# Performance work log

Hardware: AMD Instinct MI355X
Metric: run time of the kernel (lower is better)

Reference implementation:

```python
import jax, jax.numpy as jnp
import numpy as np

N, D, H, DFF, NH = 8192, 128, 256, 2048, 2
HD = D // NH
DEG = 32
E = N * DEG
LN_EPS = 1e-5


def setup_inputs() -> dict:
    key = jax.random.key(0)
    ks = jax.random.split(key, 20)
    s = 0.02
    return {
        "x": jax.random.normal(ks[0], (N, D), jnp.float32),
        "edge_index": jax.random.randint(ks[1], (2, E), 0, N, jnp.int64),
        "beta": jnp.ones((), jnp.float32),  # AGNNConv learnable beta, init 1
        "in_proj_w": jax.random.normal(ks[2], (3 * D, D), jnp.float32) * s,
        "in_proj_b": jnp.zeros((3 * D,), jnp.float32),
        "out_proj_w": jax.random.normal(ks[3], (D, D), jnp.float32) * s,
        "out_proj_b": jnp.zeros((D,), jnp.float32),
        "ln1_g": jnp.ones((D,), jnp.float32),
        "ln1_b": jnp.zeros((D,), jnp.float32),
        "ff1_w": jax.random.normal(ks[4], (DFF, D), jnp.float32) * s,
        "ff1_b": jnp.zeros((DFF,), jnp.float32),
        "ff2_w": jax.random.normal(ks[5], (D, DFF), jnp.float32) * s,
        "ff2_b": jnp.zeros((D,), jnp.float32),
        "ln2_g": jnp.ones((D,), jnp.float32),
        "ln2_b": jnp.zeros((D,), jnp.float32),
        "fc_w": jax.random.normal(ks[6], (H, D), jnp.float32) * s,
        "fc_b": jnp.zeros((H,), jnp.float32),
        "head_w": jax.random.normal(ks[7], (2, H), jnp.float32) * s,
        "head_b": jnp.zeros((2,), jnp.float32),
    }


def _layernorm(x, g, b):
    mu = jnp.mean(x, axis=-1, keepdims=True)
    var = jnp.mean((x - mu) ** 2, axis=-1, keepdims=True)
    return (x - mu) * jax.lax.rsqrt(var + LN_EPS) * g + b


def _agnn(x, edge_index, beta):
    # PyG AGNNConv: add self-loops, cosine-sim attention, segment softmax over targets
    n = x.shape[0]
    loop = jnp.arange(n, dtype=edge_index.dtype)
    src = jnp.concatenate([edge_index[0], loop])  # message source j
    dst = jnp.concatenate([edge_index[1], loop])  # aggregation target i
    xn = x / jnp.maximum(jnp.linalg.norm(x, axis=-1, keepdims=True), 1e-12)
    alpha = beta * jnp.sum(xn[dst] * xn[src], axis=-1)  # [E+N]
    m = jax.ops.segment_max(alpha, dst, num_segments=n)
    e = jnp.exp(alpha - m[dst])
    z = jax.ops.segment_sum(e, dst, num_segments=n)
    w = e / z[dst]
    return jax.ops.segment_sum(w[:, None] * x[src], dst, num_segments=n)


def reference(x, edge_index, beta, in_proj_w, in_proj_b, out_proj_w, out_proj_b,
              ln1_g, ln1_b, ff1_w, ff1_b, ff2_w, ff2_b, ln2_g, ln2_b,
              fc_w, fc_b, head_w, head_b):
    h = _agnn(x, edge_index, beta)  # [N, D]
    # transformer sees shape [N, 1, D] with batch_first=False -> seq over all N nodes
    qkv = h @ in_proj_w.T + in_proj_b  # [N, 3D]
    q, k, v = jnp.split(qkv, 3, axis=-1)
    q = q.reshape(N, NH, HD).transpose(1, 0, 2)  # [h, N, hd]
    k = k.reshape(N, NH, HD).transpose(1, 0, 2)
    v = v.reshape(N, NH, HD).transpose(1, 0, 2)
    scores = jnp.einsum('hnd,hmd->hnm', q, k) / jnp.sqrt(jnp.float32(HD))
    attn = jax.nn.softmax(scores, axis=-1)
    o = jnp.einsum('hnm,hmd->hnd', attn, v).transpose(1, 0, 2).reshape(N, D)
    o = o @ out_proj_w.T + out_proj_b
    h = _layernorm(h + o, ln1_g, ln1_b)  # post-LN (norm_first=False)
    ff = jax.nn.relu(h @ ff1_w.T + ff1_b) @ ff2_w.T + ff2_b
    h = _layernorm(h + ff, ln2_g, ln2_b)
    h = jax.nn.relu(h @ fc_w.T + fc_b)
    return h @ head_w.T + head_b  # [N, 2]
```

## Files before the change

kernel.cpp:

```cpp
#include <hip/hip_runtime.h>


typedef __attribute__((ext_vector_type(4))) float  f32x4;
typedef __attribute__((ext_vector_type(8))) __bf16 bf16x8;

#define DEV __device__ __forceinline__

DEV __bf16 f2bf(float f) {
  union { float f; unsigned u; } v; v.f = f;
  unsigned r = v.u + 0x7FFFu + ((v.u >> 16) & 1u);
  union { unsigned short s; __bf16 b; } o; o.s = (unsigned short)(r >> 16);
  return o.b;
}

DEV unsigned pk2(float a, float b) {
  union { float f; unsigned u; } x, y; x.f = a; y.f = b;
  unsigned ra = x.u + 0x7FFFu + ((x.u >> 16) & 1u);
  unsigned rb = y.u + 0x7FFFu + ((y.u >> 16) & 1u);
  return (ra >> 16) | (rb & 0xFFFF0000u);
}

DEV f32x4 mfma16(bf16x8 a, bf16x8 b, f32x4 c) {
  return __builtin_amdgcn_mfma_f32_16x16x32_bf16(a, b, c, 0, 0, 0);
}

#define GLD16(gp, lp) __builtin_amdgcn_global_load_lds(                        \
    (const __attribute__((address_space(1))) void*)(gp),                       \
    (__attribute__((address_space(3))) void*)(lp), 16, 0, 0)


__global__ __launch_bounds__(256) void k_norm(const float* __restrict__ x,
                                              float* __restrict__ inv) {
  int lane = threadIdx.x & 63, w = threadIdx.x >> 6;
  int row = blockIdx.x * 4 + w;
  float2 v = ((const float2*)(x + (size_t)row * 128))[lane];
  float s = v.x * v.x + v.y * v.y;
#pragma unroll
  for (int m = 1; m < 64; m <<= 1) s += __shfl_xor(s, m);
  if (lane == 0) inv[row] = 1.f / fmaxf(sqrtf(s), 1e-12f);
}

__global__ __launch_bounds__(256) void k_cvt5(
    const float* __restrict__ s0, const float* __restrict__ s1,
    const float* __restrict__ s2, const float* __restrict__ s3,
    const float* __restrict__ s4, __bf16* d0, __bf16* d1, __bf16* d2,
    __bf16* d3, __bf16* d4, int n0, int n1, int n2, int n3, int n4) {
  int t = blockIdx.x * 256 + threadIdx.x;
  if (t < n0) { d0[t] = f2bf(s0[t]); return; } t -= n0;
  if (t < n1) { d1[t] = f2bf(s1[t]); return; } t -= n1;
  if (t < n2) { d2[t] = f2bf(s2[t]); return; } t -= n2;
  if (t < n3) { d3[t] = f2bf(s3[t]); return; } t -= n3;
  if (t < n4) { d4[t] = f2bf(s4[t]); }
}

__global__ void k_count(const int* __restrict__ ei, int* __restrict__ counts,
                        int E) {
  int e = blockIdx.x * 256 + threadIdx.x;
  if (e < E) atomicAdd(&counts[ei[E + e]], 1);
}

__global__ __launch_bounds__(256) void k_scan(const int* __restrict__ counts,
                                              int* __restrict__ offs,
                                              int* __restrict__ cursor) {
  __shared__ int sums[256];
  int t = threadIdx.x, base = t * 32;
  int s = 0;
  for (int i = 0; i < 32; i++) s += counts[base + i];
  sums[t] = s;
  __syncthreads();
  for (int off = 1; off < 256; off <<= 1) {
    int v = (t >= off) ? sums[t - off] : 0;
    __syncthreads();
    sums[t] += v;
    __syncthreads();
  }
  int run = sums[t] - s;
  for (int i = 0; i < 32; i++) {
    offs[base + i] = run; cursor[base + i] = run;
    run += counts[base + i];
  }
  if (t == 255) offs[8192] = run;
}

__global__ void k_scatter(const int* __restrict__ ei, int* __restrict__ cursor,
                          int* __restrict__ csr, int E) {
  int e = blockIdx.x * 256 + threadIdx.x;
  if (e < E) {
    int dst = ei[E + e];
    int pos = atomicAdd(&cursor[dst], 1);
    csr[pos] = ei[e];
  }
}

__global__ __launch_bounds__(256) void k_agnn(
    const float* __restrict__ x, const int* __restrict__ csr,
    const int* __restrict__ offs, const float* __restrict__ inv,
    const float* __restrict__ betap, float* __restrict__ hf,
    __bf16* __restrict__ hb) {
  int lane = threadIdx.x & 63, w = threadIdx.x >> 6;
  int dst = blockIdx.x * 4 + w;
  float beta = *betap;
  float2 xd = ((const float2*)(x + (size_t)dst * 128))[lane];
  float invd = inv[dst];
  float sd = xd.x * xd.x + xd.y * xd.y;
#pragma unroll
  for (int m = 1; m < 64; m <<= 1) sd += __shfl_xor(sd, m);
  float z = __expf(beta * sd * invd * invd);
  float ax = z * xd.x, ay = z * xd.y;
  int e0 = offs[dst], e1 = offs[dst + 1];
  int e = e0;
  for (; e + 2 <= e1; e += 2) {
    int s0 = csr[e], s1 = csr[e + 1];
    float2 xa = ((const float2*)(x + (size_t)s0 * 128))[lane];
    float2 xb = ((const float2*)(x + (size_t)s1 * 128))[lane];
    float ia = inv[s0], ib = inv[s1];
    float da = xd.x * xa.x + xd.y * xa.y;
    float db = xd.x * xb.x + xd.y * xb.y;
#pragma unroll
    for (int m = 1; m < 64; m <<= 1) {
      da += __shfl_xor(da, m);
      db += __shfl_xor(db, m);
    }
    float sa = __expf(beta * da * invd * ia);
    float sb = __expf(beta * db * invd * ib);
    z += sa + sb;
    ax += sa * xa.x + sb * xb.x;
    ay += sa * xa.y + sb * xb.y;
  }
  if (e < e1) {
    int s0 = csr[e];
    float2 xa = ((const float2*)(x + (size_t)s0 * 128))[lane];
    float da = xd.x * xa.x + xd.y * xa.y;
#pragma unroll
    for (int m = 1; m < 64; m <<= 1) da += __shfl_xor(da, m);
    float sa = __expf(beta * da * invd * inv[s0]);
    z += sa; ax += sa * xa.x; ay += sa * xa.y;
  }
  float r = 1.f / z;
  ax *= r; ay *= r;
  float2 o; o.x = ax; o.y = ay;
  ((float2*)(hf + (size_t)dst * 128))[lane] = o;
  hb[(size_t)dst * 128 + 2 * lane]     = f2bf(ax);
  hb[(size_t)dst * 128 + 2 * lane + 1] = f2bf(ay);
}

__global__ __launch_bounds__(256, 2) void k_gemm(
    const __bf16* __restrict__ A, const __bf16* __restrict__ B,
    const float* __restrict__ bias, float* __restrict__ Cf,
    __bf16* __restrict__ Cb, float* __restrict__ Cpart, int M, int N, int K,
    int relu) {
  __shared__ __bf16 As[128 * 64];
  __shared__ __bf16 Bs[128 * 64];
  const int tid = threadIdx.x, lane = tid & 63, wid = tid >> 6;
  const int wm = wid & 1, wn = wid >> 1;
  const int bm = blockIdx.x * 128, bn = blockIdx.y * 128;
  const int kz = blockIdx.z, nkz = gridDim.z;
  const int kchunk = K / nkz, k0beg = kz * kchunk, k0end = k0beg + kchunk;
  const int lr = lane >> 3, lc8 = (lane & 7) * 8;
  const int l15 = lane & 15, quad = lane >> 4, kq = quad * 8;

  f32x4 acc[4][4] = {};
  const __bf16* Ab = A + (size_t)(bm + lr) * K + lc8;
  const __bf16* Bb = B + (size_t)(bn + lr) * K + lc8;

  for (int k0 = k0beg; k0 < k0end; k0 += 64) {
#pragma unroll
    for (int i = 0; i < 4; i++) {
      int j = wid * 4 + i;
      GLD16(Ab + (size_t)(8 * j) * K + k0, &As[j * 512]);
      GLD16(Bb + (size_t)(8 * j) * K + k0, &Bs[j * 512]);
    }
    __syncthreads();
    const int ar = (wm * 64 + l15) * 64 + kq;
    const int br = (wn * 64 + l15) * 64 + kq;
#pragma unroll
    for (int kk = 0; kk < 2; kk++) {
      bf16x8 a[4], b[4];
#pragma unroll
      for (int mt = 0; mt < 4; mt++)
        a[mt] = *(const bf16x8*)&As[ar + mt * 1024 + kk * 32];
#pragma unroll
      for (int nt = 0; nt < 4; nt++)
        b[nt] = *(const bf16x8*)&Bs[br + nt * 1024 + kk * 32];
#pragma unroll
      for (int mt = 0; mt < 4; mt++)
#pragma unroll
        for (int nt = 0; nt < 4; nt++)
          acc[mt][nt] = mfma16(a[mt], b[nt], acc[mt][nt]);
    }
    __syncthreads();
  }
  const int col0 = bn + wn * 64 + l15;
  const int row0 = bm + wm * 64 + quad * 4;
  if (Cpart) {
    float* P = Cpart + (size_t)kz * M * N;
#pragma unroll
    for (int mt = 0; mt < 4; mt++)
#pragma unroll
      for (int nt = 0; nt < 4; nt++)
#pragma unroll
        for (int r = 0; r < 4; r++)
          P[(size_t)(row0 + mt * 16 + r) * N + col0 + nt * 16] = acc[mt][nt][r];
  } else {
#pragma unroll
    for (int nt = 0; nt < 4; nt++) {
      float bv = bias[col0 + nt * 16];
#pragma unroll
      for (int mt = 0; mt < 4; mt++)
#pragma unroll
        for (int r = 0; r < 4; r++) {
          float v = acc[mt][nt][r] + bv;
          if (relu) v = fmaxf(v, 0.f);
          size_t idx = (size_t)(row0 + mt * 16 + r) * N + col0 + nt * 16;
          if (Cf) Cf[idx] = v;
          if (Cb) Cb[idx] = f2bf(v);
        }
    }
  }
}

__global__ __launch_bounds__(256) void k_qkvprep(const float* __restrict__ qkv,
                                                 __bf16* __restrict__ Qb,
                                                 __bf16* __restrict__ Kb,
                                                 __bf16* __restrict__ Vtb) {
  __shared__ __bf16 tile[64][130];
  int nb = blockIdx.x * 64;
  int t = threadIdx.x;
  for (int rr = 0; rr < 64; rr++) {
    int row = nb + rr;
    float v = qkv[(size_t)row * 384 + t];
    if (t < 128) {
      Qb[((size_t)(t >> 6) * 8192 + row) * 64 + (t & 63)] = f2bf(v * 0.125f);
    } else {
      int c = t - 128;
      Kb[((size_t)(c >> 6) * 8192 + row) * 64 + (c & 63)] = f2bf(v);
    }
  }
  int col = t & 127, rh = t >> 7;
  for (int rr = 0; rr < 64; rr += 2) {
    int row = rr + rh;
    tile[row][col] = f2bf(qkv[(size_t)(nb + row) * 384 + 256 + col]);
  }
  __syncthreads();
  int hd = t >> 1, half = t & 1;
  __bf16 tmp[32];
#pragma unroll
  for (int i = 0; i < 32; i++) tmp[i] = tile[half * 32 + i][hd];
  __bf16* dst = Vtb + (size_t)hd * 8192 + nb + half * 32;
#pragma unroll
  for (int i = 0; i < 4; i++)
    *(bf16x8*)(dst + i * 8) = *(const bf16x8*)(tmp + i * 8);
}

__global__ __launch_bounds__(256, 4) void k_attn(
    const __bf16* __restrict__ Qb, const __bf16* __restrict__ Kb,
    const __bf16* __restrict__ Vtb, float* __restrict__ Opart,
    float* __restrict__ Lpart) {
  __shared__ __bf16 Ks[4096];
  __shared__ __bf16 Vs[4096];
  __shared__ __bf16 Ps[4][32 * 88];

  const int tid = threadIdx.x, lane = tid & 63, w = tid >> 6;
  const int qt = blockIdx.x, h = blockIdx.y, kz = blockIdx.z;
  const int qbase = qt * 128;
  const int l15 = lane & 15, quad = lane >> 4;
  const int lofs = lane * 8;

  const __bf16* Qg = Qb + ((size_t)h * 8192 + qbase) * 64;
  const __bf16* Kg = Kb + (size_t)h * 8192 * 64;
  const __bf16* Vg = Vtb + (size_t)h * 64 * 8192;

#pragma unroll
  for (int i = 0; i < 2; i++) {
    int j = w * 2 + i;
    __bf16* dstb = (j < 4) ? &Ks[j * 1024] : &Vs[(j - 4) * 1024];
#pragma unroll
    for (int hh = 0; hh < 2; hh++)
      GLD16(Qg + (size_t)(j * 16 + l15) * 64 + hh * 32 + quad * 8,
            dstb + hh * 512);
  }
  __syncthreads();
  bf16x8 aq[2][2];
#pragma unroll
  for (int s = 0; s < 2; s++) {
    int j = w * 2 + s;
    const __bf16* base = (j < 4) ? &Ks[j * 1024] : &Vs[(j - 4) * 1024];
    aq[s][0] = *(const bf16x8*)&base[lofs];
    aq[s][1] = *(const bf16x8*)&base[512 + lofs];
  }
  __syncthreads();

  f32x4 o[2][4] = {};
  float lsum[2] = {0.f, 0.f};
  const int kstart = kz * 1024;

  for (int kt = 0; kt < 16; kt++) {
    int kb = kstart + kt * 64;
#pragma unroll
    for (int hh = 0; hh < 2; hh++) {
      GLD16(Kg + (size_t)(kb + w * 16 + l15) * 64 + hh * 32 + quad * 8,
            &Ks[w * 1024 + hh * 512]);
      GLD16(Vg + (size_t)(w * 16 + l15) * 8192 + kb + hh * 32 + quad * 8,
            &Vs[w * 1024 + hh * 512]);
    }
    __syncthreads();

#pragma unroll
    for (int mt = 0; mt < 4; mt++) {
      bf16x8 k0 = *(const bf16x8*)&Ks[mt * 1024 + lofs];
      bf16x8 k1 = *(const bf16x8*)&Ks[mt * 1024 + 512 + lofs];
#pragma unroll
      for (int s = 0; s < 2; s++) {
        f32x4 St = {};
        St = mfma16(k0, aq[s][0], St);
        St = mfma16(k1, aq[s][1], St);
        float p0 = __expf(St[0]), p1 = __expf(St[1]);
        float p2 = __expf(St[2]), p3 = __expf(St[3]);
        lsum[s] += (p0 + p1) + (p2 + p3);
        uint2 pk;
        pk.x = pk2(p0, p1);
        pk.y = pk2(p2, p3);
        *(uint2*)&Ps[w][(s * 16 + l15) * 88 + mt * 16 + quad * 4] = pk;
      }
    }
#pragma unroll
    for (int s = 0; s < 2; s++) {
      bf16x8 ap0 = *(const bf16x8*)&Ps[w][(s * 16 + l15) * 88 + quad * 8];
      bf16x8 ap1 = *(const bf16x8*)&Ps[w][(s * 16 + l15) * 88 + 32 + quad * 8];
#pragma unroll
      for (int nd = 0; nd < 4; nd++) {
        bf16x8 v0 = *(const bf16x8*)&Vs[nd * 1024 + lofs];
        bf16x8 v1 = *(const bf16x8*)&Vs[nd * 1024 + 512 + lofs];
        o[s][nd] = mfma16(ap0, v0, o[s][nd]);
        o[s][nd] = mfma16(ap1, v1, o[s][nd]);
      }
    }
    __syncthreads();
  }

#pragma unroll
  for (int s = 0; s < 2; s++) {
    float v = lsum[s];
    v += __shfl_xor(v, 16);
    v += __shfl_xor(v, 32);
    lsum[s] = v;
  }

  const size_t bpart = (size_t)(h * 8 + kz);
#pragma unroll
  for (int s = 0; s < 2; s++) {
#pragma unroll
    for (int nd = 0; nd < 4; nd++)
#pragma unroll
      for (int r = 0; r < 4; r++) {
        int row = qbase + w * 32 + s * 16 + quad * 4 + r;
        Opart[(bpart * 8192 + row) * 64 + nd * 16 + l15] = o[s][nd][r];
      }
    if (lane < 16) {
      int row = qbase + w * 32 + s * 16 + l15;
      Lpart[bpart * 8192 + row] = lsum[s];
    }
  }
}

__global__ __launch_bounds__(256) void k_attn_combine(
    const float* __restrict__ Opart, const float* __restrict__ Lpart,
    __bf16* __restrict__ obf) {
  int t = blockIdx.x * 256 + threadIdx.x;
  int d = t & 63;
  int n = (t >> 6) & 8191;
  int h = t >> 19;
  float acc = 0.f, L = 0.f;
#pragma unroll
  for (int z = 0; z < 8; z++) {
    size_t idx = (size_t)(h * 8 + z) * 8192 + n;
    acc += Opart[idx * 64 + d];
    L += Lpart[idx];
  }
  obf[(size_t)n * 128 + h * 64 + d] = f2bf(acc / L);
}

__global__ __launch_bounds__(256) void k_addln(
    const float* __restrict__ A, const float* __restrict__ Bv,
    const float* __restrict__ g, const float* __restrict__ bt,
    float* __restrict__ outf, __bf16* __restrict__ outb) {
  int lane = threadIdx.x & 63, w = threadIdx.x >> 6;
  int row = blockIdx.x * 4 + w;
  float2 a = ((const float2*)(A + (size_t)row * 128))[lane];
  float2 b = ((const float2*)(Bv + (size_t)row * 128))[lane];
  float vx = a.x + b.x, vy = a.y + b.y;
  float s = vx + vy;
#pragma unroll
  for (int m = 1; m < 64; m <<= 1) s += __shfl_xor(s, m);
  float mu = s * (1.f / 128.f);
  float dx = vx - mu, dy = vy - mu;
  float q = dx * dx + dy * dy;
#pragma unroll
  for (int m = 1; m < 64; m <<= 1) q += __shfl_xor(q, m);
  float rstd = rsqrtf(q * (1.f / 128.f) + 1e-5f);
  float2 gg = ((const float2*)g)[lane];
  float2 bb = ((const float2*)bt)[lane];
  float y0 = dx * rstd * gg.x + bb.x;
  float y1 = dy * rstd * gg.y + bb.y;
  if (outf) {
    float2 o; o.x = y0; o.y = y1;
    ((float2*)(outf + (size_t)row * 128))[lane] = o;
  }
  if (outb) {
    outb[(size_t)row * 128 + 2 * lane]     = f2bf(y0);
    outb[(size_t)row * 128 + 2 * lane + 1] = f2bf(y1);
  }
}

__global__ __launch_bounds__(256) void k_addln4(
    const float* __restrict__ A, const float* __restrict__ part,
    const float* __restrict__ pbias, const float* __restrict__ g,
    const float* __restrict__ bt, __bf16* __restrict__ outb) {
  int lane = threadIdx.x & 63, w = threadIdx.x >> 6;
  int row = blockIdx.x * 4 + w;
  float2 a = ((const float2*)(A + (size_t)row * 128))[lane];
  float2 pb = ((const float2*)pbias)[lane];
  float sx = 0.f, sy = 0.f;
#pragma unroll
  for (int z = 0; z < 4; z++) {
    float2 p =
        ((const float2*)(part + (size_t)z * 1048576 + (size_t)row * 128))[lane];
    sx += p.x; sy += p.y;
  }
  float vx = a.x + pb.x + sx, vy = a.y + pb.y + sy;
  float s = vx + vy;
#pragma unroll
  for (int m = 1; m < 64; m <<= 1) s += __shfl_xor(s, m);
  float mu = s * (1.f / 128.f);
  float dx = vx - mu, dy = vy - mu;
  float q = dx * dx + dy * dy;
#pragma unroll
  for (int m = 1; m < 64; m <<= 1) q += __shfl_xor(q, m);
  float rstd = rsqrtf(q * (1.f / 128.f) + 1e-5f);
  float2 gg = ((const float2*)g)[lane];
  float2 bb = ((const float2*)bt)[lane];
  outb[(size_t)row * 128 + 2 * lane]     = f2bf(dx * rstd * gg.x + bb.x);
  outb[(size_t)row * 128 + 2 * lane + 1] = f2bf(dy * rstd * gg.y + bb.y);
}

__global__ __launch_bounds__(256) void k_head(const float* __restrict__ fc,
                                              const float* __restrict__ hw,
                                              const float* __restrict__ hb,
                                              float* __restrict__ out) {
  int lane = threadIdx.x & 63, w = threadIdx.x >> 6;
  int row = blockIdx.x * 4 + w;
  float4 v  = ((const float4*)(fc + (size_t)row * 256))[lane];
  float4 w0 = ((const float4*)hw)[lane];
  float4 w1 = ((const float4*)(hw + 256))[lane];
  float p0 = v.x * w0.x + v.y * w0.y + v.z * w0.z + v.w * w0.w;
  float p1 = v.x * w1.x + v.y * w1.y + v.z * w1.z + v.w * w1.w;
#pragma unroll
  for (int m = 1; m < 64; m <<= 1) {
    p0 += __shfl_xor(p0, m);
    p1 += __shfl_xor(p1, m);
  }
  if (lane == 0) {
    out[(size_t)row * 2]     = p0 + hb[0];
    out[(size_t)row * 2 + 1] = p1 + hb[1];
  }
}

extern "C" void kernel_launch(void* const* d_in, const int* in_sizes, int n_in,
                              void* d_out, int out_size, void* d_ws,
                              size_t ws_size, hipStream_t stream) {
  const float* x     = (const float*)d_in[0];
  const int*   ei    = (const int*)d_in[1];
  const float* beta  = (const float*)d_in[2];
  const float* in_w  = (const float*)d_in[3];
  const float* in_b  = (const float*)d_in[4];
  const float* out_w = (const float*)d_in[5];
  const float* out_b = (const float*)d_in[6];
  const float* ln1g  = (const float*)d_in[7];
  const float* ln1b  = (const float*)d_in[8];
  const float* ff1w  = (const float*)d_in[9];
  const float* ff1b  = (const float*)d_in[10];
  const float* ff2w  = (const float*)d_in[11];
  const float* ff2b  = (const float*)d_in[12];
  const float* ln2g  = (const float*)d_in[13];
  const float* ln2b  = (const float*)d_in[14];
  const float* fcw   = (const float*)d_in[15];
  const float* fcb   = (const float*)d_in[16];
  const float* hw    = (const float*)d_in[17];
  const float* hbias = (const float*)d_in[18];
  float* out = (float*)d_out;
  const int N = 8192;
  const int E = in_sizes[1] / 2;

  char* wsp = (char*)d_ws;
  size_t off = 0;
  auto alloc = [&](size_t b) -> void* {
    void* p = wsp + off;
    off = (off + b + 255) & ~(size_t)255;
    return p;
  };

  float*  inv     = (float*)alloc((size_t)N * 4);
  int*    counts  = (int*)alloc((size_t)N * 4);
  int*    offs    = (int*)alloc((size_t)(N + 1) * 4);
  int*    cursor  = (int*)alloc((size_t)N * 4);
  int*    csr     = (int*)alloc((size_t)E * 4);
  float*  h_f     = (float*)alloc((size_t)N * 128 * 4);
  __bf16* h_b     = (__bf16*)alloc((size_t)N * 128 * 2);
  __bf16* o_b     = (__bf16*)alloc((size_t)N * 128 * 2);
  float*  oproj   = (float*)alloc((size_t)N * 128 * 4);
  float*  h1_f    = (float*)alloc((size_t)N * 128 * 4);
  __bf16* h1_b    = (__bf16*)alloc((size_t)N * 128 * 2);
  __bf16* h2_b    = (__bf16*)alloc((size_t)N * 128 * 2);
  float*  fco     = (float*)alloc((size_t)N * 256 * 4);
  float*  Lpart   = (float*)alloc((size_t)16 * N * 4);
  __bf16* w_in    = (__bf16*)alloc((size_t)384 * 128 * 2);
  __bf16* w_out   = (__bf16*)alloc((size_t)128 * 128 * 2);
  __bf16* w_ff1   = (__bf16*)alloc((size_t)2048 * 128 * 2);
  __bf16* w_ff2   = (__bf16*)alloc((size_t)128 * 2048 * 2);
  __bf16* w_fc    = (__bf16*)alloc((size_t)256 * 128 * 2);
  char*   bigA    = (char*)alloc((size_t)16 * N * 64 * 4);
  float*  Opart   = (float*)bigA;
  __bf16* ff1o    = (__bf16*)bigA;
  char*   bigB    = (char*)alloc((size_t)18874368);
  float*  qkv     = (float*)bigB;
  __bf16* Qb      = (__bf16*)(bigB + 12582912);
  __bf16* Kb      = (__bf16*)(bigB + 12582912 + 2097152);
  __bf16* Vtb     = (__bf16*)(bigB + 12582912 + 2 * 2097152);
  float*  ff2part = (float*)bigB;
  (void)ws_size; (void)n_in; (void)out_size;

  hipMemsetAsync(counts, 0, (size_t)N * 4, stream);
  k_norm<<<N / 4, 256, 0, stream>>>(x, inv);
  {
    int n0 = 384 * 128, n1 = 128 * 128, n2 = 2048 * 128, n3 = 128 * 2048,
        n4 = 256 * 128;
    int tot = n0 + n1 + n2 + n3 + n4;
    k_cvt5<<<(tot + 255) / 256, 256, 0, stream>>>(
        in_w, out_w, ff1w, ff2w, fcw, w_in, w_out, w_ff1, w_ff2, w_fc, n0, n1,
        n2, n3, n4);
  }
  k_count<<<(E + 255) / 256, 256, 0, stream>>>(ei, counts, E);
  k_scan<<<1, 256, 0, stream>>>(counts, offs, cursor);
  k_scatter<<<(E + 255) / 256, 256, 0, stream>>>(ei, cursor, csr, E);
  k_agnn<<<N / 4, 256, 0, stream>>>(x, csr, offs, inv, beta, h_f, h_b);

  k_gemm<<<dim3(64, 3, 1), 256, 0, stream>>>(h_b, w_in, in_b, qkv, nullptr,
                                             nullptr, N, 384, 128, 0);
  k_qkvprep<<<128, 256, 0, stream>>>(qkv, Qb, Kb, Vtb);
  k_attn<<<dim3(64, 2, 8), 256, 0, stream>>>(Qb, Kb, Vtb, Opart, Lpart);
  k_attn_combine<<<(2 * N * 64) / 256, 256, 0, stream>>>(Opart, Lpart, o_b);
  k_gemm<<<dim3(64, 1, 1), 256, 0, stream>>>(o_b, w_out, out_b, oproj, nullptr,
                                             nullptr, N, 128, 128, 0);
  k_addln<<<N / 4, 256, 0, stream>>>(h_f, oproj, ln1g, ln1b, h1_f, h1_b);
  k_gemm<<<dim3(64, 16, 1), 256, 0, stream>>>(h1_b, w_ff1, ff1b, nullptr, ff1o,
                                              nullptr, N, 2048, 128, 1);
  k_gemm<<<dim3(64, 1, 4), 256, 0, stream>>>(ff1o, w_ff2, nullptr, nullptr,
                                             nullptr, ff2part, N, 128, 2048, 0);
  k_addln4<<<N / 4, 256, 0, stream>>>(h1_f, ff2part, ff2b, ln2g, ln2b, h2_b);
  k_gemm<<<dim3(64, 2, 1), 256, 0, stream>>>(h2_b, w_fc, fcb, fco, nullptr,
                                             nullptr, N, 256, 128, 1);
  k_head<<<N / 4, 256, 0, stream>>>(fco, hw, hbias, out);
}
```

Baseline: 299.6 us.

## Use exp2 softmax, MFMA row sums, truncating bf16 pack, and bf16 partial outputs

Result: faster. 287.2 us (-4.1%).

```diff
diff --git a/kernel.cpp b/kernel.cpp
--- a/kernel.cpp
+++ b/kernel.cpp
@@ -13,15 +13,15 @@
   return o.b;
 }
 
-DEV unsigned pk2(float a, float b) {
-  union { float f; unsigned u; } x, y; x.f = a; y.f = b;
-  unsigned ra = x.u + 0x7FFFu + ((x.u >> 16) & 1u);
-  unsigned rb = y.u + 0x7FFFu + ((y.u >> 16) & 1u);
-  return (ra >> 16) | (rb & 0xFFFF0000u);
-}
-
 DEV f32x4 mfma16(bf16x8 a, bf16x8 b, f32x4 c) {
   return __builtin_amdgcn_mfma_f32_16x16x32_bf16(a, b, c, 0, 0, 0);
+}
+
+DEV bf16x8 ones8() {
+  union { unsigned short s[8]; bf16x8 v; } u;
+#pragma unroll
+  for (int i = 0; i < 8; i++) u.s[i] = 0x3F80;
+  return u.v;
 }
 
 #define GLD16(gp, lp) __builtin_amdgcn_global_load_lds(                        \
@@ -226,11 +226,12 @@
   __shared__ __bf16 tile[64][130];
   int nb = blockIdx.x * 64;
   int t = threadIdx.x;
+  const float qscale = 0.125f * 1.44269504089f;
   for (int rr = 0; rr < 64; rr++) {
     int row = nb + rr;
     float v = qkv[(size_t)row * 384 + t];
     if (t < 128) {
-      Qb[((size_t)(t >> 6) * 8192 + row) * 64 + (t & 63)] = f2bf(v * 0.125f);
+      Qb[((size_t)(t >> 6) * 8192 + row) * 64 + (t & 63)] = f2bf(v * qscale);
     } else {
       int c = t - 128;
       Kb[((size_t)(c >> 6) * 8192 + row) * 64 + (c & 63)] = f2bf(v);
@@ -254,7 +255,7 @@
 
 __global__ __launch_bounds__(256, 4) void k_attn(
     const __bf16* __restrict__ Qb, const __bf16* __restrict__ Kb,
-    const __bf16* __restrict__ Vtb, float* __restrict__ Opart,
+    const __bf16* __restrict__ Vtb, __bf16* __restrict__ Opart,
     float* __restrict__ Lpart) {
   __shared__ __bf16 Ks[4096];
   __shared__ __bf16 Vs[4096];
@@ -269,6 +270,7 @@
   const __bf16* Qg = Qb + ((size_t)h * 8192 + qbase) * 64;
   const __bf16* Kg = Kb + (size_t)h * 8192 * 64;
   const __bf16* Vg = Vtb + (size_t)h * 64 * 8192;
+  const bf16x8 vone = ones8();
 
 #pragma unroll
   for (int i = 0; i < 2; i++) {
@@ -291,7 +293,7 @@
   __syncthreads();
 
   f32x4 o[2][4] = {};
-  float lsum[2] = {0.f, 0.f};
+  f32x4 lacc[2] = {};
   const int kstart = kz * 1024;
 
   for (int kt = 0; kt < 16; kt++) {
@@ -314,36 +316,36 @@
         f32x4 St = {};
         St = mfma16(k0, aq[s][0], St);
         St = mfma16(k1, aq[s][1], St);
-        float p0 = __expf(St[0]), p1 = __expf(St[1]);
-        float p2 = __expf(St[2]), p3 = __expf(St[3]);
-        lsum[s] += (p0 + p1) + (p2 + p3);
+        union { float f; unsigned u; } p0, p1, p2, p3;
+        p0.f = __builtin_amdgcn_exp2f(St[0]);
+        p1.f = __builtin_amdgcn_exp2f(St[1]);
+        p2.f = __builtin_amdgcn_exp2f(St[2]);
+        p3.f = __builtin_amdgcn_exp2f(St[3]);
         uint2 pk;
-        pk.x = pk2(p0, p1);
-        pk.y = pk2(p2, p3);
+        pk.x = (p0.u >> 16) | (p1.u & 0xFFFF0000u);
+        pk.y = (p2.u >> 16) | (p3.u & 0xFFFF0000u);
         *(uint2*)&Ps[w][(s * 16 + l15) * 88 + mt * 16 + quad * 4] = pk;
       }
+    }
+    bf16x8 vf[4][2];
+#pragma unroll
+    for (int nd = 0; nd < 4; nd++) {
+      vf[nd][0] = *(const bf16x8*)&Vs[nd * 1024 + lofs];
+      vf[nd][1] = *(const bf16x8*)&Vs[nd * 1024 + 512 + lofs];
     }
 #pragma unroll
     for (int s = 0; s < 2; s++) {
       bf16x8 ap0 = *(const bf16x8*)&Ps[w][(s * 16 + l15) * 88 + quad * 8];
       bf16x8 ap1 = *(const bf16x8*)&Ps[w][(s * 16 + l15) * 88 + 32 + quad * 8];
+      lacc[s] = mfma16(ap0, vone, lacc[s]);
+      lacc[s] = mfma16(ap1, vone, lacc[s]);
 #pragma unroll
       for (int nd = 0; nd < 4; nd++) {
-        bf16x8 v0 = *(const bf16x8*)&Vs[nd * 1024 + lofs];
-        bf16x8 v1 = *(const bf16x8*)&Vs[nd * 1024 + 512 + lofs];
-        o[s][nd] = mfma16(ap0, v0, o[s][nd]);
-        o[s][nd] = mfma16(ap1, v1, o[s][nd]);
+        o[s][nd] = mfma16(ap0, vf[nd][0], o[s][nd]);
+        o[s][nd] = mfma16(ap1, vf[nd][1], o[s][nd]);
       }
     }
     __syncthreads();
-  }
-
-#pragma unroll
-  for (int s = 0; s < 2; s++) {
-    float v = lsum[s];
-    v += __shfl_xor(v, 16);
-    v += __shfl_xor(v, 32);
-    lsum[s] = v;
   }
 
   const size_t bpart = (size_t)(h * 8 + kz);
@@ -354,17 +356,20 @@
 #pragma unroll
       for (int r = 0; r < 4; r++) {
         int row = qbase + w * 32 + s * 16 + quad * 4 + r;
-        Opart[(bpart * 8192 + row) * 64 + nd * 16 + l15] = o[s][nd][r];
+        Opart[(bpart * 8192 + row) * 64 + nd * 16 + l15] = f2bf(o[s][nd][r]);
       }
-    if (lane < 16) {
-      int row = qbase + w * 32 + s * 16 + l15;
-      Lpart[bpart * 8192 + row] = lsum[s];
+    if (l15 == 0) {
+#pragma unroll
+      for (int r = 0; r < 4; r++) {
+        int row = qbase + w * 32 + s * 16 + quad * 4 + r;
+        Lpart[bpart * 8192 + row] = lacc[s][r];
+      }
     }
   }
 }
 
 __global__ __launch_bounds__(256) void k_attn_combine(
-    const float* __restrict__ Opart, const float* __restrict__ Lpart,
+    const __bf16* __restrict__ Opart, const float* __restrict__ Lpart,
     __bf16* __restrict__ obf) {
   int t = blockIdx.x * 256 + threadIdx.x;
   int d = t & 63;
@@ -374,7 +379,7 @@
 #pragma unroll
   for (int z = 0; z < 8; z++) {
     size_t idx = (size_t)(h * 8 + z) * 8192 + n;
-    acc += Opart[idx * 64 + d];
+    acc += (float)Opart[idx * 64 + d];
     L += Lpart[idx];
   }
   obf[(size_t)n * 128 + h * 64 + d] = f2bf(acc / L);
@@ -519,7 +524,7 @@
   __bf16* w_ff2   = (__bf16*)alloc((size_t)128 * 2048 * 2);
   __bf16* w_fc    = (__bf16*)alloc((size_t)256 * 128 * 2);
   char*   bigA    = (char*)alloc((size_t)16 * N * 64 * 4);
-  float*  Opart   = (float*)bigA;
+  __bf16* Opart   = (__bf16*)bigA;
   __bf16* ff1o    = (__bf16*)bigA;
   char*   bigB    = (char*)alloc((size_t)18874368);
   float*  qkv     = (float*)bigB;
```
